# Kernel tuning notes

Hardware: AMD Instinct MI355X
Metric: run time of the kernel (lower is better)

Reference implementation:

```python
import jax, jax.numpy as jnp
import numpy as np

B, C, N, H = 4, 256, 4096, 4
DK = C // H


def _proj(x, w, b):
    # Conv1d with kernel size 1 == per-point linear: [B,C,N] x [O,C] -> [B,O,N]
    return jnp.einsum('oc,bcn->bon', w, x) + b[None, :, None]


def setup_inputs() -> dict:
    key = jax.random.key(0)
    ks = jax.random.split(key, 9)
    s = 1.0 / np.sqrt(C)
    return {
        'x': jax.random.normal(ks[0], (B, C, N), jnp.float32),
        'wq': jax.random.normal(ks[1], (C, C), jnp.float32) * s,
        'bq': jax.random.normal(ks[2], (C,), jnp.float32) * 0.01,
        'wk': jax.random.normal(ks[3], (C, C), jnp.float32) * s,
        'bk': jax.random.normal(ks[4], (C,), jnp.float32) * 0.01,
        'wv': jax.random.normal(ks[5], (C, C), jnp.float32) * s,
        'bv': jax.random.normal(ks[6], (C,), jnp.float32) * 0.01,
        'wp': jax.random.normal(ks[7], (C, C), jnp.float32) * s,
        'bp': jax.random.normal(ks[8], (C,), jnp.float32) * 0.01,
    }


def reference(x, wq, bq, wk, bk, wv, bv, wp, bp):
    b, c, n = x.shape
    q = _proj(x, wq, bq).reshape(b, H, DK, n)
    k = _proj(x, wk, bk).reshape(b, H, DK, n)
    v = _proj(x, wv, bv).reshape(b, H, DK, n)
    scale = 1.0 / jnp.sqrt(jnp.asarray(DK, x.dtype))
    # scores over point pairs: [B,H,N,N]
    scores = jnp.einsum('bhdn,bhdm->bhnm', q, k) * scale
    attn = jax.nn.softmax(scores, axis=-1)
    out = jnp.einsum('bhnm,bhdm->bhdn', attn, v)  # [B,H,DK,N]
    out = out.reshape(b, c, n)
    out = _proj(out, wp, bp)
    return out + x
```

## Files before the change

kernel.cpp:

```cpp
#include <hip/hip_runtime.h>


#define BDIM 4
#define CDIM 256
#define NDIM 4096
#define HDIM 4
#define DKDIM 64
#define NQ   (BDIM * HDIM * NDIM)
#define NSPLIT 2
#define KPERZ (NDIM / NSPLIT)
#define QSCALE 0.18033688011112042f
#define WSZ (CDIM * CDIM)

typedef __bf16 bf16x8 __attribute__((ext_vector_type(8)));
typedef float f32x4 __attribute__((ext_vector_type(4)));
typedef short s16x4 __attribute__((ext_vector_type(4)));
typedef unsigned short u16;
typedef unsigned int u32;

__device__ __forceinline__ u16 f2bf(float f) {
  union { __bf16 h; u16 s; } u; u.h = (__bf16)f; return u.s;
}
__device__ __forceinline__ float bf2f(u16 v) {
  union { u32 u; float f; } x; x.u = (u32)v << 16; return x.f;
}
__device__ __forceinline__ u32 pk2(float a, float b) {
  return (u32)f2bf(a) | ((u32)f2bf(b) << 16);
}
__device__ __forceinline__ void gload16(const u16* g, u16* l) {
  __builtin_amdgcn_global_load_lds(
      (const __attribute__((address_space(1))) void*)g,
      (__attribute__((address_space(3))) void*)l, 16, 0, 0);
}

__global__ __launch_bounds__(256) void wconv_kernel(
    const float* __restrict__ wq, const float* __restrict__ wk,
    const float* __restrict__ wv, const float* __restrict__ wp,
    u16* __restrict__ wb)
{
  const int a = blockIdx.y;
  const float* src = (a == 0) ? wq : (a == 1) ? wk : (a == 2) ? wv : wp;
  const float sc = (a == 0) ? QSCALE : 1.0f;
  const int i = (blockIdx.x * 256 + threadIdx.x) * 8;
  const float4 v0 = *(const float4*)(src + i);
  const float4 v1 = *(const float4*)(src + i + 4);
  union { u32 p[4]; uint4 q; } o;
  o.p[0] = pk2(v0.x * sc, v0.y * sc);
  o.p[1] = pk2(v0.z * sc, v0.w * sc);
  o.p[2] = pk2(v1.x * sc, v1.y * sc);
  o.p[3] = pk2(v1.z * sc, v1.w * sc);
  *(uint4*)(wb + (size_t)a * WSZ + i) = o.q;
}

__global__ __launch_bounds__(256) void xt_kernel(
    const float* __restrict__ x, u16* __restrict__ xT)
{
  const int b = blockIdx.z, c0 = blockIdx.y * 64, n0 = blockIdx.x * 64;
  __shared__ __align__(16) float T[64][68];
  const int t = threadIdx.x;
  {
    const int cr = t >> 4, nc = (t & 15) * 4;
    #pragma unroll
    for (int ci = 0; ci < 4; ++ci) {
      const float4 v = *(const float4*)&x[((size_t)(b * CDIM + c0 + cr + ci * 16)) * NDIM + n0 + nc];
      *(float4*)&T[cr + ci * 16][nc] = v;
    }
  }
  __syncthreads();
  {
    const int n = t >> 2, g = t & 3;
    union { u16 u[16]; uint4 v[2]; } pk;
    #pragma unroll
    for (int u_ = 0; u_ < 16; ++u_) pk.u[u_] = f2bf(T[g * 16 + u_][n]);
    uint4* dst = (uint4*)&xT[((size_t)(b * NDIM + n0 + n)) * CDIM + c0 + g * 16];
    dst[0] = pk.v[0]; dst[1] = pk.v[1];
  }
}

__global__ __launch_bounds__(256, 4) void qkv_kernel(
    const u16* __restrict__ xT, const u16* __restrict__ wb,
    const float* __restrict__ bq, const float* __restrict__ bk,
    const float* __restrict__ bv,
    u16* __restrict__ qT, u16* __restrict__ kT, u16* __restrict__ vB)
{
  const int b = blockIdx.z;
  const int p = blockIdx.y >> 1;
  const int o0 = (blockIdx.y & 1) * 128;
  const int n0 = blockIdx.x * 64;
  const float* bsel = (p == 0) ? bq : (p == 1) ? bk : bv;
  const float wscale = (p == 0) ? QSCALE : 1.0f;

  __shared__ __align__(16) u16 XTs[64][264];
  const int t = threadIdx.x, lane = t & 63, w = t >> 6;
  const int qd = lane >> 4, lm = lane & 15;
  const int sr = t >> 2, sg = (t & 3) * 8;

  {
    const u16* xsrc = xT + ((size_t)(b * NDIM + n0 + sr)) * CDIM + sg;
    #pragma unroll
    for (int cs = 0; cs < 8; ++cs)
      *(uint4*)&XTs[sr][cs * 32 + sg] = *(const uint4*)(xsrc + cs * 32);
  }
  __syncthreads();

  const u16* wrow0 = wb + (size_t)p * WSZ + (size_t)(o0 + 32 * w + lm) * CDIM + qd * 8;
  const u16* wrow1 = wrow0 + (size_t)16 * CDIM;

  f32x4 acc[4][2];
  #pragma unroll
  for (int nt = 0; nt < 4; ++nt)
    #pragma unroll
    for (int j = 0; j < 2; ++j) acc[nt][j] = (f32x4){0.f, 0.f, 0.f, 0.f};

  #pragma unroll
  for (int cs = 0; cs < 8; ++cs) {
    const bf16x8 wf0 = *(const bf16x8*)(wrow0 + cs * 32);
    const bf16x8 wf1 = *(const bf16x8*)(wrow1 + cs * 32);
    bf16x8 xf[4];
    #pragma unroll
    for (int nt = 0; nt < 4; ++nt)
      xf[nt] = *(const bf16x8*)&XTs[16 * nt + lm][cs * 32 + qd * 8];
    #pragma unroll
    for (int nt = 0; nt < 4; ++nt) {
      if (p < 2) {
        acc[nt][0] = __builtin_amdgcn_mfma_f32_16x16x32_bf16(xf[nt], wf0, acc[nt][0], 0, 0, 0);
        acc[nt][1] = __builtin_amdgcn_mfma_f32_16x16x32_bf16(xf[nt], wf1, acc[nt][1], 0, 0, 0);
      } else {
        acc[nt][0] = __builtin_amdgcn_mfma_f32_16x16x32_bf16(wf0, xf[nt], acc[nt][0], 0, 0, 0);
        acc[nt][1] = __builtin_amdgcn_mfma_f32_16x16x32_bf16(wf1, xf[nt], acc[nt][1], 0, 0, 0);
      }
    }
  }

  if (p < 2) {
    u16* out = (p == 0) ? qT : kT;
    #pragma unroll
    for (int j = 0; j < 2; ++j) {
      const int og = o0 + 32 * w + 16 * j + lm;
      const float bv2 = bsel[og] * wscale;
      #pragma unroll
      for (int nt = 0; nt < 4; ++nt)
        #pragma unroll
        for (int r = 0; r < 4; ++r) {
          const int n = n0 + 16 * nt + 4 * qd + r;
          out[((size_t)(b * NDIM + n)) * CDIM + og] = f2bf(acc[nt][j][r] + bv2);
        }
    }
  } else {
    #pragma unroll
    for (int j = 0; j < 2; ++j) {
      const float4 b4 = *(const float4*)&bsel[o0 + 32 * w + 16 * j + 4 * qd];
      const float bvr[4] = {b4.x, b4.y, b4.z, b4.w};
      #pragma unroll
      for (int nt = 0; nt < 4; ++nt)
        #pragma unroll
        for (int r = 0; r < 4; ++r) {
          const int og = o0 + 32 * w + 16 * j + 4 * qd + r;
          const int n = n0 + 16 * nt + lm;
          vB[((size_t)(b * CDIM + og)) * NDIM + n] = f2bf(acc[nt][j][r] + bvr[r]);
        }
    }
  }
}

__global__ __launch_bounds__(1024, 2) void attn_kernel(
    const u16* __restrict__ qT, const u16* __restrict__ kT,
    const u16* __restrict__ vB, u16* __restrict__ Opart,
    float* __restrict__ Lp)
{
  const int bh = blockIdx.y, b = bh >> 2, h = bh & 3;
  const int n0 = blockIdx.x * 512;
  const int z  = blockIdx.z;

  struct SH { u16 K[2][64][64]; u16 V[2][64][72]; };
  __shared__ __align__(16) SH sh;

  const int t = threadIdx.x, lane = t & 63, w = t >> 6;
  const int qd = lane >> 4, lm = lane & 15, l7 = lm & 7;

  bf16x8 qf[2][2];
  {
    const u16* qbase = qT + ((size_t)(b * NDIM) + n0) * CDIM + h * 64;
    #pragma unroll
    for (int s = 0; s < 2; ++s)
      #pragma unroll
      for (int hh = 0; hh < 2; ++hh)
        qf[s][hh] = *(const bf16x8*)(qbase +
            (size_t)(16 * (2 * w + s) + lm) * CDIM + 32 * hh + qd * 8);
  }

  const s16x4 ones = (s16x4){(short)0x3F80, (short)0x3F80, (short)0x3F80, (short)0x3F80};
  f32x4 la[2];
  la[0] = (f32x4){0.f, 0.f, 0.f, 0.f};
  la[1] = (f32x4){0.f, 0.f, 0.f, 0.f};

  f32x4 oa[2][4];
  #pragma unroll
  for (int s = 0; s < 2; ++s)
    #pragma unroll
    for (int dt = 0; dt < 4; ++dt) oa[s][dt] = (f32x4){0.f, 0.f, 0.f, 0.f};

  const int sw = w & 7;
  const int r8 = lane >> 3, l8 = lane & 7;
  const int kswz = 8 * (l8 ^ r8);
  const u16* kp0 = kT + ((size_t)(b * NDIM + z * KPERZ + 8 * sw + r8)) * CDIM + h * 64 + kswz;
  const u16* vp0 = vB + ((size_t)(b * CDIM + h * 64 + 8 * sw + r8)) * NDIM + z * KPERZ + 8 * l8;

  if (w < 8) {
    gload16(kp0, &sh.K[0][0][0] + sw * 512);
  } else {
    const uint4 v0 = *(const uint4*)(vp0);
    *(uint4*)&sh.V[0][8 * sw + r8][8 * l8] = v0;
  }

  uint4 vreg;
  #pragma unroll 1
  for (int it = 0; it < KPERZ / 64; ++it) {
    __syncthreads();
    const bool pf = (it + 1 < KPERZ / 64);
    if (pf) {
      if (w < 8) {
        gload16(kp0 + (size_t)(it + 1) * 64 * CDIM,
                &sh.K[(it + 1) & 1][0][0] + sw * 512);
      } else {
        vreg = *(const uint4*)(vp0 + (it + 1) * 64);
      }
    }
    const u16 (*Kt)[64] = sh.K[it & 1];
    const u16 (*Vt)[72] = sh.V[it & 1];

    union { u16 u[4]; u32 d[2]; s16x4 v; } pk[2][4];

    #pragma unroll
    for (int nt = 0; nt < 4; ++nt) {
      const bf16x8 kf0 = *(const bf16x8*)&Kt[16 * nt + lm][8 * (qd ^ l7)];
      const bf16x8 kf1 = *(const bf16x8*)&Kt[16 * nt + lm][8 * ((4 + qd) ^ l7)];
      #pragma unroll
      for (int s = 0; s < 2; ++s) {
        f32x4 zz = (f32x4){0.f, 0.f, 0.f, 0.f};
        zz = __builtin_amdgcn_mfma_f32_16x16x32_bf16(kf0, qf[s][0], zz, 0, 0, 0);
        zz = __builtin_amdgcn_mfma_f32_16x16x32_bf16(kf1, qf[s][1], zz, 0, 0, 0);
        const float p0 = __builtin_amdgcn_exp2f(zz[0]);
        const float p1 = __builtin_amdgcn_exp2f(zz[1]);
        const float p2 = __builtin_amdgcn_exp2f(zz[2]);
        const float p3 = __builtin_amdgcn_exp2f(zz[3]);
        pk[s][nt].d[0] = pk2(p0, p1);
        pk[s][nt].d[1] = pk2(p2, p3);
      }
    }

    #pragma unroll
    for (int c = 0; c < 4; ++c) {
      s16x4 av[4];
      #pragma unroll
      for (int dt = 0; dt < 4; ++dt)
        av[dt] = *(const s16x4*)&Vt[16 * dt + lm][16 * c + 4 * qd];
      la[0] = __builtin_amdgcn_mfma_f32_16x16x16bf16_1k(ones, pk[0][c].v, la[0], 0, 0, 0);
      la[1] = __builtin_amdgcn_mfma_f32_16x16x16bf16_1k(ones, pk[1][c].v, la[1], 0, 0, 0);
      #pragma unroll
      for (int dt = 0; dt < 4; ++dt) {
        oa[0][dt] = __builtin_amdgcn_mfma_f32_16x16x16bf16_1k(av[dt], pk[0][c].v, oa[0][dt], 0, 0, 0);
        oa[1][dt] = __builtin_amdgcn_mfma_f32_16x16x16bf16_1k(av[dt], pk[1][c].v, oa[1][dt], 0, 0, 0);
      }
    }

    if (pf && w >= 8)
      *(uint4*)&sh.V[(it + 1) & 1][8 * sw + r8][8 * l8] = vreg;
  }

  const float l_i[2] = {la[0][0], la[1][0]};

  if (qd == 0) {
    const size_t lbase = ((size_t)z * (BDIM * HDIM) + bh) * NDIM;
    #pragma unroll
    for (int s = 0; s < 2; ++s)
      Lp[lbase + n0 + 16 * (2 * w + s) + lm] = l_i[s];
  }

  __syncthreads();
  u16 (*Ot)[72] = (u16(*)[72])&sh.K[0][0][0];
  #pragma unroll
  for (int ph = 0; ph < 4; ++ph) {
    if ((w >> 2) == ph) {
      const int wl = w & 3;
      #pragma unroll
      for (int s = 0; s < 2; ++s) {
        const float inv = 1.0f / l_i[s];
        #pragma unroll
        for (int dt = 0; dt < 4; ++dt)
          #pragma unroll
          for (int r = 0; r < 4; ++r)
            Ot[16 * (2 * wl + s) + lm][16 * dt + 4 * qd + r] = f2bf(oa[s][dt][r] * inv);
      }
    }
    __syncthreads();
    {
      const int r = t >> 3, g = (t & 7) * 8;
      u16* dst = Opart + (((size_t)z * (BDIM * HDIM) + bh) * NDIM + n0 + ph * 128 + r) * DKDIM + g;
      *(uint4*)dst = *(const uint4*)&Ot[r][g];
    }
    __syncthreads();
  }
}

__global__ __launch_bounds__(256, 4) void projout_kernel(
    const u16* __restrict__ Opart, const float* __restrict__ Lp,
    const u16* __restrict__ wb, const float* __restrict__ bp,
    const float* __restrict__ res, float* __restrict__ out)
{
  const int b = blockIdx.z, o0 = blockIdx.y * 128, n0 = blockIdx.x * 64;
  __shared__ __align__(16) u16 XTs[64][40];
  const int t = threadIdx.x, lane = t & 63, w = t >> 6;
  const int qd = lane >> 4, lm = lane & 15;
  const int sr = t >> 2, sg = (t & 3) * 8;

  float wh[4][NSPLIT];
  #pragma unroll
  for (int hh = 0; hh < 4; ++hh) {
    const size_t i0 = ((size_t)(b * HDIM + hh)) * NDIM + n0 + sr;
    float l[NSPLIT], tot = 0.f;
    #pragma unroll
    for (int zz = 0; zz < NSPLIT; ++zz) { l[zz] = Lp[(size_t)zz * NQ + i0]; tot += l[zz]; }
    const float iv = 1.0f / tot;
    #pragma unroll
    for (int zz = 0; zz < NSPLIT; ++zz) wh[hh][zz] = l[zz] * iv;
  }

  const u16* wrow0 = wb + (size_t)3 * WSZ + (size_t)(o0 + 32 * w + lm) * CDIM + qd * 8;
  const u16* wrow1 = wrow0 + (size_t)16 * CDIM;

  f32x4 acc[4][2];
  #pragma unroll
  for (int nt = 0; nt < 4; ++nt)
    #pragma unroll
    for (int j = 0; j < 2; ++j) acc[nt][j] = (f32x4){0.f, 0.f, 0.f, 0.f};

  for (int cs = 0; cs < 8; ++cs) {
    const int c0 = cs * 32;
    const int hh = c0 >> 6;
    const int dk = (c0 & 63) + sg;
    const bf16x8 wf0 = *(const bf16x8*)(wrow0 + c0);
    const bf16x8 wf1 = *(const bf16x8*)(wrow1 + c0);
    __syncthreads();
    {
      const size_t obase = (((size_t)(b * HDIM + hh)) * NDIM + n0 + sr) * DKDIM + dk;
      float v[8] = {0.f, 0.f, 0.f, 0.f, 0.f, 0.f, 0.f, 0.f};
      #pragma unroll
      for (int zz = 0; zz < NSPLIT; ++zz) {
        union { u16 u[8]; uint4 q; } a;
        a.q = *(const uint4*)(Opart + (size_t)zz * NQ * DKDIM + obase);
        const float wz = wh[hh][zz];
        #pragma unroll
        for (int j = 0; j < 8; ++j) v[j] = fmaf(wz, bf2f(a.u[j]), v[j]);
      }
      union { u16 u[8]; uint4 q; } ov;
      #pragma unroll
      for (int j = 0; j < 8; ++j) ov.u[j] = f2bf(v[j]);
      *(uint4*)&XTs[sr][sg] = ov.q;
    }
    __syncthreads();
    bf16x8 xf[4];
    #pragma unroll
    for (int nt = 0; nt < 4; ++nt) xf[nt] = *(const bf16x8*)&XTs[16 * nt + lm][qd * 8];
    #pragma unroll
    for (int nt = 0; nt < 4; ++nt) {
      acc[nt][0] = __builtin_amdgcn_mfma_f32_16x16x32_bf16(wf0, xf[nt], acc[nt][0], 0, 0, 0);
      acc[nt][1] = __builtin_amdgcn_mfma_f32_16x16x32_bf16(wf1, xf[nt], acc[nt][1], 0, 0, 0);
    }
  }

  #pragma unroll
  for (int j = 0; j < 2; ++j) {
    const float4 b4 = *(const float4*)&bp[o0 + 32 * w + 16 * j + 4 * qd];
    const float bvr[4] = {b4.x, b4.y, b4.z, b4.w};
    #pragma unroll
    for (int nt = 0; nt < 4; ++nt)
      #pragma unroll
      for (int r = 0; r < 4; ++r) {
        const int og = o0 + 32 * w + 16 * j + 4 * qd + r;
        const int n = n0 + 16 * nt + lm;
        const size_t idx = ((size_t)(b * CDIM + og)) * NDIM + n;
        out[idx] = acc[nt][j][r] + bvr[r] + res[idx];
      }
  }
}

extern "C" void kernel_launch(void* const* d_in, const int* in_sizes, int n_in,
                              void* d_out, int out_size, void* d_ws, size_t ws_size,
                              hipStream_t stream)
{
  const float* x  = (const float*)d_in[0];
  const float* wq = (const float*)d_in[1];
  const float* bq = (const float*)d_in[2];
  const float* wk = (const float*)d_in[3];
  const float* bk = (const float*)d_in[4];
  const float* wv = (const float*)d_in[5];
  const float* bv = (const float*)d_in[6];
  const float* wp = (const float*)d_in[7];
  const float* bp = (const float*)d_in[8];
  float* out = (float*)d_out;

  const size_t sz = (size_t)BDIM * CDIM * NDIM;
  u16* xTb = (u16*)d_ws;
  u16* qTb = xTb + sz;
  u16* kTb = qTb + sz;
  u16* vBb = kTb + sz;
  u16* Opart = vBb + sz;
  float* Lp = (float*)(Opart + (size_t)NSPLIT * sz);
  u16* wbf = (u16*)(Lp + (size_t)NSPLIT * NQ);

  const dim3 blk(256);
  wconv_kernel<<<dim3(WSZ / (256 * 8), 4, 1), blk, 0, stream>>>(wq, wk, wv, wp, wbf);
  xt_kernel<<<dim3(NDIM / 64, CDIM / 64, BDIM), blk, 0, stream>>>(x, xTb);
  qkv_kernel<<<dim3(NDIM / 64, 6, BDIM), blk, 0, stream>>>(
      xTb, wbf, bq, bk, bv, qTb, kTb, vBb);
  attn_kernel<<<dim3(NDIM / 512, BDIM * HDIM, NSPLIT), dim3(1024), 0, stream>>>(
      qTb, kTb, vBb, Opart, Lp);
  projout_kernel<<<dim3(NDIM / 64, 2, BDIM), blk, 0, stream>>>(
      Opart, Lp, wbf, bp, x, out);
}
```

Measured before the change: 195.5 us.

## Double KV tile to 128 keys and load V via async global-to-LDS with swizzle

```diff
diff --git a/kernel.cpp b/kernel.cpp
--- a/kernel.cpp
+++ b/kernel.cpp
@@ -172,7 +172,7 @@
   const int n0 = blockIdx.x * 512;
   const int z  = blockIdx.z;
 
-  struct SH { u16 K[2][64][64]; u16 V[2][64][72]; };
+  struct SH { u16 K[2][128][64]; u16 V[2][64][128]; };
   __shared__ __align__(16) SH sh;
 
   const int t = threadIdx.x, lane = t & 63, w = t >> 6;
@@ -202,37 +202,42 @@
 
   const int sw = w & 7;
   const int r8 = lane >> 3, l8 = lane & 7;
-  const int kswz = 8 * (l8 ^ r8);
-  const u16* kp0 = kT + ((size_t)(b * NDIM + z * KPERZ + 8 * sw + r8)) * CDIM + h * 64 + kswz;
-  const u16* vp0 = vB + ((size_t)(b * CDIM + h * 64 + 8 * sw + r8)) * NDIM + z * KPERZ + 8 * l8;
+  const u16* kpA = kT + ((size_t)(b * NDIM + z * KPERZ + 16 * sw + r8)) * CDIM + h * 64 + 8 * (l8 ^ r8);
+  const u16* kpB = kpA + (size_t)8 * CDIM;
+  const int r4 = lane >> 4, g16 = lane & 15;
+  const u16* vpA = vB + ((size_t)(b * CDIM + h * 64 + 8 * sw + r4)) * NDIM + z * KPERZ + 8 * (g16 ^ (r4 & 7));
+  const u16* vpB = vB + ((size_t)(b * CDIM + h * 64 + 8 * sw + 4 + r4)) * NDIM + z * KPERZ + 8 * (g16 ^ ((4 + r4) & 7));
 
   if (w < 8) {
-    gload16(kp0, &sh.K[0][0][0] + sw * 512);
+    gload16(kpA, &sh.K[0][16 * sw][0]);
+    gload16(kpB, &sh.K[0][16 * sw + 8][0]);
   } else {
-    const uint4 v0 = *(const uint4*)(vp0);
-    *(uint4*)&sh.V[0][8 * sw + r8][8 * l8] = v0;
-  }
-
-  uint4 vreg;
+    gload16(vpA, &sh.V[0][8 * sw][0]);
+    gload16(vpB, &sh.V[0][8 * sw + 4][0]);
+  }
+
   #pragma unroll 1
-  for (int it = 0; it < KPERZ / 64; ++it) {
+  for (int it = 0; it < KPERZ / 128; ++it) {
     __syncthreads();
-    const bool pf = (it + 1 < KPERZ / 64);
-    if (pf) {
+    if (it + 1 < KPERZ / 128) {
+      const int nb = (it + 1) & 1;
       if (w < 8) {
-        gload16(kp0 + (size_t)(it + 1) * 64 * CDIM,
-                &sh.K[(it + 1) & 1][0][0] + sw * 512);
+        const size_t ko = (size_t)(it + 1) * 128 * CDIM;
+        gload16(kpA + ko, &sh.K[nb][16 * sw][0]);
+        gload16(kpB + ko, &sh.K[nb][16 * sw + 8][0]);
       } else {
-        vreg = *(const uint4*)(vp0 + (it + 1) * 64);
-      }
-    }
-    const u16 (*Kt)[64] = sh.K[it & 1];
-    const u16 (*Vt)[72] = sh.V[it & 1];
-
-    union { u16 u[4]; u32 d[2]; s16x4 v; } pk[2][4];
-
-    #pragma unroll
-    for (int nt = 0; nt < 4; ++nt) {
+        const int vo = (it + 1) * 128;
+        gload16(vpA + vo, &sh.V[nb][8 * sw][0]);
+        gload16(vpB + vo, &sh.V[nb][8 * sw + 4][0]);
+      }
+    }
+    const u16 (*Kt)[64]  = sh.K[it & 1];
+    const u16 (*Vt)[128] = sh.V[it & 1];
+
+    union { u16 u[4]; u32 d[2]; s16x4 v; } pk[2][8];
+
+    #pragma unroll
+    for (int nt = 0; nt < 8; ++nt) {
       const bf16x8 kf0 = *(const bf16x8*)&Kt[16 * nt + lm][8 * (qd ^ l7)];
       const bf16x8 kf1 = *(const bf16x8*)&Kt[16 * nt + lm][8 * ((4 + qd) ^ l7)];
       #pragma unroll
@@ -250,11 +255,11 @@
     }
 
     #pragma unroll
-    for (int c = 0; c < 4; ++c) {
+    for (int c = 0; c < 8; ++c) {
       s16x4 av[4];
       #pragma unroll
       for (int dt = 0; dt < 4; ++dt)
-        av[dt] = *(const s16x4*)&Vt[16 * dt + lm][16 * c + 4 * qd];
+        av[dt] = *(const s16x4*)&Vt[16 * dt + lm][(16 * c + 4 * qd) ^ (8 * l7)];
       la[0] = __builtin_amdgcn_mfma_f32_16x16x16bf16_1k(ones, pk[0][c].v, la[0], 0, 0, 0);
       la[1] = __builtin_amdgcn_mfma_f32_16x16x16bf16_1k(ones, pk[1][c].v, la[1], 0, 0, 0);
       #pragma unroll
@@ -263,9 +268,6 @@
         oa[1][dt] = __builtin_amdgcn_mfma_f32_16x16x16bf16_1k(av[dt], pk[1][c].v, oa[1][dt], 0, 0, 0);
       }
     }
-
-    if (pf && w >= 8)
-      *(uint4*)&sh.V[(it + 1) & 1][8 * sw + r8][8 * l8] = vreg;
   }
 
   const float l_i[2] = {la[0][0], la[1][0]};
```

New measurement: 197.4 us. About the same (+1.0%).
